# Kernel optimization log

Hardware: AMD Instinct MI355X
Metric: run time of the kernel (lower is better)

## Reference

```python
import jax, jax.numpy as jnp
import numpy as np

N = 30000      # nodes
E = 480000     # edges (before self-loops)
IN = 128       # in_dim
HID = 256      # hidden_dim
HEADS = 4
C = HID // HEADS  # per-head channels = 64
NEG_SLOPE = 0.2


def setup_inputs() -> dict:
    key = jax.random.key(0)
    ks = jax.random.split(key, 12)
    s_in = 1.0 / np.sqrt(IN)
    s_h = 1.0 / np.sqrt(HID)
    return {
        "x": jax.random.normal(ks[0], (N, IN), dtype=jnp.float32),
        "edge_index": jax.random.randint(ks[1], (2, E), 0, N, dtype=jnp.int32),
        # GAT layer 1 (in: IN -> HEADS*C)
        "W1": jax.random.normal(ks[2], (IN, HID), dtype=jnp.float32) * s_in,
        "att_src1": jax.random.normal(ks[3], (HEADS, C), dtype=jnp.float32) * s_h,
        "att_dst1": jax.random.normal(ks[4], (HEADS, C), dtype=jnp.float32) * s_h,
        "b1": jnp.zeros((HID,), dtype=jnp.float32),
        # GAT layer 2 (in: HID -> HEADS*C)
        "W2": jax.random.normal(ks[5], (HID, HID), dtype=jnp.float32) * s_h,
        "att_src2": jax.random.normal(ks[6], (HEADS, C), dtype=jnp.float32) * s_h,
        "att_dst2": jax.random.normal(ks[7], (HEADS, C), dtype=jnp.float32) * s_h,
        "b2": jnp.zeros((HID,), dtype=jnp.float32),
        # LayerNorms
        "g1": jnp.ones((HID,), dtype=jnp.float32),
        "be1": jnp.zeros((HID,), dtype=jnp.float32),
        "g2": jnp.ones((HID,), dtype=jnp.float32),
        "be2": jnp.zeros((HID,), dtype=jnp.float32),
        # residual projection (in_dim != hidden_dim)
        "Wp": jax.random.normal(ks[8], (IN, HID), dtype=jnp.float32) * s_in,
        "bp": jnp.zeros((HID,), dtype=jnp.float32),
    }


def layer_norm(x, g, b, eps=1e-5):
    mu = jnp.mean(x, axis=-1, keepdims=True)
    var = jnp.var(x, axis=-1, keepdims=True)
    return (x - mu) * jax.lax.rsqrt(var + eps) * g + b


def gat_conv(x, src, dst, W, a_src, a_dst, bias):
    """PyG-style GATConv (concat heads). src/dst already include self-loops."""
    n = x.shape[0]
    h = (x @ W).reshape(n, HEADS, C)                     # (N, H, C)
    e_src = jnp.sum(h * a_src, axis=-1)                  # (N, H)
    e_dst = jnp.sum(h * a_dst, axis=-1)                  # (N, H)
    e = jax.nn.leaky_relu(e_src[src] + e_dst[dst], NEG_SLOPE)  # (Etot, H)
    # per-destination segment softmax (numerically stable)
    e_max = jax.lax.stop_gradient(jax.ops.segment_max(e, dst, num_segments=n))
    p = jnp.exp(e - e_max[dst])
    denom = jax.ops.segment_sum(p, dst, num_segments=n)[dst]
    alpha = p / denom                                    # (Etot, H)
    out = jax.ops.segment_sum(h[src] * alpha[..., None], dst, num_segments=n)
    return out.reshape(n, HID) + bias


def reference(x, edge_index, W1, att_src1, att_dst1, b1, W2, att_src2, att_dst2, b2,
              g1, be1, g2, be2, Wp, bp):
    n = x.shape[0]
    loop = jnp.arange(n, dtype=edge_index.dtype)
    src = jnp.concatenate([edge_index[0], loop])
    dst = jnp.concatenate([edge_index[1], loop])

    residual = x @ Wp + bp                               # proj residual
    h = gat_conv(x, src, dst, W1, att_src1, att_dst1, b1)
    h = jax.nn.elu(layer_norm(h + residual, g1, be1))
    # dropout is identity at inference
    residual = h
    h2 = gat_conv(h, src, dst, W2, att_src2, att_dst2, b2)
    out = jax.nn.elu(layer_norm(h2 + residual, g2, be2))
    return out
```

## Files before the change

kernel.cpp:

```cpp
#include <hip/hip_runtime.h>
#include <cstdint>
#include <cstddef>

#define N_NODES 30000
#define E_EDGES 480000
#define ETOT    510000
#define IN_DIM  128
#define HID     256
#define HEADS   4
#define NEG_SLOPE 0.2f
#define DEG_BLOCKS 1993

static inline int cdiv(int a, int b){ return (a + b - 1) / b; }

typedef short bf16x8 __attribute__((ext_vector_type(8)));
typedef float f32x4  __attribute__((ext_vector_type(4)));
typedef float f32x2  __attribute__((ext_vector_type(2)));

__device__ __forceinline__ unsigned short f2bf(float f) {
  unsigned u = __float_as_uint(f);
  unsigned r = (u + 0x7FFFu + ((u >> 16) & 1u)) >> 16;
  return (unsigned short)r;
}
__device__ __forceinline__ float bf2f(unsigned short s) {
  return __uint_as_float((unsigned)s << 16);
}
__device__ __forceinline__ unsigned char f2fp8(float v) {
  return (unsigned char)(__builtin_amdgcn_cvt_pk_fp8_f32(v, v, 0, false) & 0xFF);
}

__global__ __launch_bounds__(256) void zero_deg(int4* __restrict__ deg4)
{
  deg4[blockIdx.x * 256 + threadIdx.x] = int4{0, 0, 0, 0};
}

__global__ __launch_bounds__(256) void setup(
    const int* __restrict__ ei, int* __restrict__ deg,
    const float* __restrict__ x, const float* __restrict__ W1,
    const float* __restrict__ Wp, const float* __restrict__ W2,
    ushort* __restrict__ xbf, ushort* __restrict__ w1t,
    ushort* __restrict__ wpt, ushort* __restrict__ w2t)
{
  int b = blockIdx.x;
  int t = threadIdx.x;
  if (b < DEG_BLOCKS) {
    int e = b * 256 + t;
    if (e < ETOT) {
      int d = (e < E_EDGES) ? ei[E_EDGES + e] : (e - E_EDGES);
      atomicAdd(&deg[d], 1);
    }
    return;
  }
  b -= DEG_BLOCKS;
  if (b < 3750) {
    int i = b * 256 + t;
    float4 v = ((const float4*)x)[i];
    ushort4 o;
    o.x = f2bf(v.x); o.y = f2bf(v.y); o.z = f2bf(v.z); o.w = f2bf(v.w);
    ((ushort4*)xbf)[i] = o;
  } else if (b < 3750 + 128) {
    int k = b - 3750;
    w1t[(size_t)t * IN_DIM + k] = f2bf(W1[(size_t)k * HID + t]);
  } else if (b < 3750 + 256) {
    int k = b - 3878;
    wpt[(size_t)t * IN_DIM + k] = f2bf(Wp[(size_t)k * HID + t]);
  } else {
    int k = b - 4006;
    w2t[(size_t)t * HID + k] = f2bf(W2[(size_t)k * HID + t]);
  }
}

template<int K, bool L1>
__global__ __launch_bounds__(256) void gemm_fused(
    const ushort* __restrict__ A,
    const ushort* __restrict__ WT,
    const float* __restrict__ att_src, const float* __restrict__ att_dst,
    unsigned char* __restrict__ hout, float* __restrict__ esrc, float* __restrict__ edst,
    ushort* __restrict__ rout, const float* __restrict__ pbias, int n)
{
  const int wave = threadIdx.x >> 6;
  const int lane = threadIdx.x & 63;
  const int wr = wave >> 1, wc = wave & 1;
  const int brow = blockIdx.x * 128 + wr * 64;
  const int bcol = blockIdx.y * 128 + wc * 64;
  const int lrow = lane & 15;
  const int kgrp = lane >> 4;

  f32x4 acc[4][4] = {};
  for (int k0 = 0; k0 < K; k0 += 32) {
    const int kb = k0 + kgrp * 8;
    bf16x8 a[4], b[4];
    #pragma unroll
    for (int mi = 0; mi < 4; ++mi) {
      int r = brow + mi * 16 + lrow;
      r = min(r, n - 1);
      a[mi] = *(const bf16x8*)&A[(size_t)r * K + kb];
    }
    #pragma unroll
    for (int ni = 0; ni < 4; ++ni) {
      int c = bcol + ni * 16 + lrow;
      b[ni] = *(const bf16x8*)&WT[(size_t)c * K + kb];
    }
    #pragma unroll
    for (int mi = 0; mi < 4; ++mi)
      #pragma unroll
      for (int ni = 0; ni < 4; ++ni)
        acc[mi][ni] = __builtin_amdgcn_mfma_f32_16x16x32_bf16(a[mi], b[ni], acc[mi][ni], 0, 0, 0);
  }
  const bool proj = L1 && (bcol >= 256);
  #pragma unroll
  for (int mi = 0; mi < 4; ++mi) {
    #pragma unroll
    for (int r = 0; r < 4; ++r) {
      int row = brow + mi * 16 + kgrp * 4 + r;
      if (row < n) {
        #pragma unroll
        for (int ni = 0; ni < 4; ++ni) {
          int colg = bcol + ni * 16 + lrow;
          float v = acc[mi][ni][r];
          if (proj) {
            int c = colg - 256;
            rout[(size_t)row * HID + c] = f2bf(v + pbias[c]);
          } else {
            hout[(size_t)row * HID + colg] = f2fp8(v);
          }
        }
      }
    }
  }
  if (!proj) {
    const int hh = bcol >> 6;
    float as[4], ad[4];
    #pragma unroll
    for (int ni = 0; ni < 4; ++ni) {
      as[ni] = att_src[hh * 64 + ni * 16 + lrow];
      ad[ni] = att_dst[hh * 64 + ni * 16 + lrow];
    }
    #pragma unroll
    for (int mi = 0; mi < 4; ++mi) {
      #pragma unroll
      for (int r = 0; r < 4; ++r) {
        float vs = 0.f, vd = 0.f;
        #pragma unroll
        for (int ni = 0; ni < 4; ++ni) {
          float c = acc[mi][ni][r];
          vs += c * as[ni];
          vd += c * ad[ni];
        }
        #pragma unroll
        for (int m = 1; m <= 8; m <<= 1) {
          vs += __shfl_xor(vs, m);
          vd += __shfl_xor(vd, m);
        }
        int row = brow + mi * 16 + kgrp * 4 + r;
        if (lrow == 0 && row < n) {
          esrc[row * HEADS + hh] = vs;
          edst[row * HEADS + hh] = vd;
        }
      }
    }
  }
}

__global__ __launch_bounds__(1024) void scan_rowptr(const int* __restrict__ deg,
                                                    int* __restrict__ rowptr,
                                                    int* __restrict__ cursor)
{
  const int CE = 30;
  __shared__ int sc[1024];
  int t = threadIdx.x;
  int base = t * CE;
  int local[CE];
  int s = 0;
  #pragma unroll
  for (int i = 0; i < CE; ++i) {
    int idx = base + i;
    int v = (idx < N_NODES) ? deg[idx] : 0;
    local[i] = s;
    s += v;
  }
  sc[t] = s;
  __syncthreads();
  for (int o = 1; o < 1024; o <<= 1) {
    int v = (t >= o) ? sc[t - o] : 0;
    __syncthreads();
    sc[t] += v;
    __syncthreads();
  }
  int off = sc[t] - s;
  #pragma unroll
  for (int i = 0; i < CE; ++i) {
    int idx = base + i;
    if (idx < N_NODES) {
      rowptr[idx] = off + local[i];
      cursor[idx] = off + local[i];
    }
  }
  if (t == 1023) rowptr[N_NODES] = off + s;
}

__global__ __launch_bounds__(256) void scatter_edges(const int* __restrict__ ei,
                                                     int* __restrict__ cursor,
                                                     int* __restrict__ col)
{
  int e = blockIdx.x * blockDim.x + threadIdx.x;
  if (e >= ETOT) return;
  int s, d;
  if (e < E_EDGES) { s = ei[e]; d = ei[E_EDGES + e]; }
  else             { s = d = e - E_EDGES; }
  int pos = atomicAdd(&cursor[d], 1);
  col[pos] = s;
}

template<bool WRITE_BF16>
__global__ __launch_bounds__(256) void gat_agg(
    const int* __restrict__ rowptr, const int* __restrict__ col,
    const float* __restrict__ esrc, const float* __restrict__ edst,
    const unsigned char* __restrict__ h8, const float* __restrict__ bias,
    const ushort* __restrict__ resid, const float* __restrict__ gamma,
    const float* __restrict__ beta, float* __restrict__ out_f32,
    ushort* __restrict__ out_bf16)
{
  const int t = threadIdx.x;
  const int lane16 = t & 15;
  const int d = blockIdx.x * 16 + (t >> 4);
  const int cblk = lane16 * 16;
  const int headc = lane16 >> 2;
  const int r0 = rowptr[d], r1 = rowptr[d + 1];

  const float edh = edst[d * HEADS + headc];
  f32x2 acc2[8] = {};
  float dp = 0.f;

  for (int j = r0; j < r1; j += 8) {
    int s[8];
    #pragma unroll
    for (int i = 0; i < 8; ++i) s[i] = col[min(j + i, r1 - 1)];
    float es[8];
    #pragma unroll
    for (int i = 0; i < 8; ++i) es[i] = esrc[s[i] * HEADS + headc];
    uint4 w[8];
    #pragma unroll
    for (int i = 0; i < 8; ++i)
      w[i] = *(const uint4*)&h8[(size_t)s[i] * HID + cblk];
    #pragma unroll
    for (int i = 0; i < 8; ++i) {
      float v = es[i] + edh;
      v = (v >= 0.f) ? v : NEG_SLOPE * v;
      float p = (j + i < r1) ? __expf(v) : 0.f;
      dp += p;
      f32x2 p2 = { p, p };
      unsigned wd0 = w[i].x, wd1 = w[i].y, wd2 = w[i].z, wd3 = w[i].w;
      acc2[0] += __builtin_amdgcn_cvt_pk_f32_fp8(wd0, false) * p2;
      acc2[1] += __builtin_amdgcn_cvt_pk_f32_fp8(wd0, true)  * p2;
      acc2[2] += __builtin_amdgcn_cvt_pk_f32_fp8(wd1, false) * p2;
      acc2[3] += __builtin_amdgcn_cvt_pk_f32_fp8(wd1, true)  * p2;
      acc2[4] += __builtin_amdgcn_cvt_pk_f32_fp8(wd2, false) * p2;
      acc2[5] += __builtin_amdgcn_cvt_pk_f32_fp8(wd2, true)  * p2;
      acc2[6] += __builtin_amdgcn_cvt_pk_f32_fp8(wd3, false) * p2;
      acc2[7] += __builtin_amdgcn_cvt_pk_f32_fp8(wd3, true)  * p2;
    }
  }

  float rden = 1.f / dp;

  f32x2 v2[8];
  {
    const uint4* rp = (const uint4*)&resid[(size_t)d * HID + cblk];
    uint4 r0v = rp[0], r1v = rp[1];
    unsigned rd[8] = { r0v.x, r0v.y, r0v.z, r0v.w, r1v.x, r1v.y, r1v.z, r1v.w };
    const f32x2* b2 = (const f32x2*)&bias[cblk];
    f32x2 rden2 = { rden, rden };
    #pragma unroll
    for (int q = 0; q < 8; ++q) {
      f32x2 rw;
      rw.x = __uint_as_float(rd[q] << 16);
      rw.y = __uint_as_float(rd[q] & 0xffff0000u);
      v2[q] = acc2[q] * rden2 + b2[q] + rw;
    }
  }

  float s1 = 0.f, s2 = 0.f;
  #pragma unroll
  for (int q = 0; q < 8; ++q) {
    s1 += v2[q].x + v2[q].y;
    s2 += v2[q].x * v2[q].x + v2[q].y * v2[q].y;
  }
  #pragma unroll
  for (int m = 1; m <= 8; m <<= 1) {
    s1 += __shfl_xor(s1, m);
    s2 += __shfl_xor(s2, m);
  }
  float mu = s1 * (1.f / HID);
  float var = s2 * (1.f / HID) - mu * mu;
  float rr = rsqrtf(var + 1e-5f);

  const f32x2* g2 = (const f32x2*)&gamma[cblk];
  const f32x2* e2 = (const f32x2*)&beta[cblk];
  float y[16];
  #pragma unroll
  for (int q = 0; q < 8; ++q) {
    f32x2 g = g2[q], e = e2[q];
    float t0 = (v2[q].x - mu) * rr * g.x + e.x;
    float t1 = (v2[q].y - mu) * rr * g.y + e.y;
    y[2 * q]     = (t0 > 0.f) ? t0 : expm1f(t0);
    y[2 * q + 1] = (t1 > 0.f) ? t1 : expm1f(t1);
  }
  if (WRITE_BF16) {
    uint4 o[2];
    #pragma unroll
    for (int q = 0; q < 8; ++q) {
      unsigned wv = (unsigned)f2bf(y[2 * q]) | ((unsigned)f2bf(y[2 * q + 1]) << 16);
      ((unsigned*)o)[q] = wv;
    }
    uint4* op = (uint4*)&out_bf16[(size_t)d * HID + cblk];
    op[0] = o[0]; op[1] = o[1];
  } else {
    float4* op = (float4*)&out_f32[(size_t)d * HID + cblk];
    #pragma unroll
    for (int q = 0; q < 4; ++q) {
      float4 ov = { y[4 * q], y[4 * q + 1], y[4 * q + 2], y[4 * q + 3] };
      op[q] = ov;
    }
  }
}

extern "C" void kernel_launch(void* const* d_in, const int* in_sizes, int n_in,
                              void* d_out, int out_size, void* d_ws, size_t ws_size,
                              hipStream_t stream) {
  const float* x   = (const float*)d_in[0];
  const int*   ei  = (const int*)d_in[1];
  const float* W1  = (const float*)d_in[2];
  const float* as1 = (const float*)d_in[3];
  const float* ad1 = (const float*)d_in[4];
  const float* b1  = (const float*)d_in[5];
  const float* W2  = (const float*)d_in[6];
  const float* as2 = (const float*)d_in[7];
  const float* ad2 = (const float*)d_in[8];
  const float* b2  = (const float*)d_in[9];
  const float* g1  = (const float*)d_in[10];
  const float* be1 = (const float*)d_in[11];
  const float* g2  = (const float*)d_in[12];
  const float* be2 = (const float*)d_in[13];
  const float* Wp  = (const float*)d_in[14];
  const float* bp  = (const float*)d_in[15];
  float* out = (float*)d_out;

  const size_t NB16 = (size_t)N_NODES * HID * sizeof(ushort);
  const size_t NB8  = (size_t)N_NODES * HID;
  const size_t XB16 = (size_t)N_NODES * IN_DIM * sizeof(ushort);
  const size_t NH_BUF = (size_t)N_NODES * HEADS * sizeof(float);
  char* ws = (char*)d_ws;
  size_t off = 0;
  unsigned char* h8 = (unsigned char*)(ws + off); off += NB8;
  ushort* hAbf  = (ushort*)(ws + off); off += NB16;
  ushort* rbf   = (ushort*)(ws + off); off += NB16;
  ushort* xbf   = (ushort*)(ws + off); off += XB16;
  ushort* w1t   = (ushort*)(ws + off); off += (size_t)HID * IN_DIM * 2;
  ushort* wpt   = (ushort*)(ws + off); off += (size_t)HID * IN_DIM * 2;
  ushort* w2t   = (ushort*)(ws + off); off += (size_t)HID * HID * 2;
  float*  esrc  = (float*) (ws + off); off += NH_BUF;
  float*  edstb = (float*) (ws + off); off += NH_BUF;
  int*    deg    = (int*)(ws + off); off += (size_t)30720 * 4;
  int*    rowptr = (int*)(ws + off); off += (size_t)(N_NODES + 1) * 4;
  int*    cursor = (int*)(ws + off); off += (size_t)N_NODES * 4;
  int*    col    = (int*)(ws + off); off += (size_t)ETOT * 4;

  zero_deg<<<30, 256, 0, stream>>>((int4*)deg);
  setup<<<DEG_BLOCKS + 3750 + 128 + 128 + 256, 256, 0, stream>>>(
      ei, deg, x, W1, Wp, W2, xbf, w1t, wpt, w2t);
  scan_rowptr<<<1, 1024, 0, stream>>>(deg, rowptr, cursor);
  scatter_edges<<<cdiv(ETOT, 256), 256, 0, stream>>>(ei, cursor, col);

  gemm_fused<IN_DIM, true><<<dim3(cdiv(N_NODES, 128), 4), 256, 0, stream>>>(
      xbf, w1t, as1, ad1, h8, esrc, edstb, rbf, bp, N_NODES);
  gat_agg<true><<<N_NODES / 16, 256, 0, stream>>>(
      rowptr, col, esrc, edstb, h8, b1, rbf, g1, be1, nullptr, hAbf);

  gemm_fused<HID, false><<<dim3(cdiv(N_NODES, 128), 2), 256, 0, stream>>>(
      hAbf, w2t, as2, ad2, h8, esrc, edstb, nullptr, nullptr, N_NODES);
  gat_agg<false><<<N_NODES / 16, 256, 0, stream>>>(
      rowptr, col, esrc, edstb, h8, b2, hAbf, g2, be2, out, nullptr);
}
```

Measured before the change: 218.3 us.

## Fuse edge scatter into first GEMM launch, warp-shuffle scan, hoist residual load

```diff
diff --git a/kernel.cpp b/kernel.cpp
--- a/kernel.cpp
+++ b/kernel.cpp
@@ -10,6 +10,7 @@
 #define HEADS   4
 #define NEG_SLOPE 0.2f
 #define DEG_BLOCKS 1993
+#define GEMM1_BX 235
 
 static inline int cdiv(int a, int b){ return (a + b - 1) / b; }
 
@@ -71,7 +72,8 @@
 }
 
 template<int K, bool L1>
-__global__ __launch_bounds__(256) void gemm_fused(
+__device__ __forceinline__ void gemm_body(
+    int bx, int by,
     const ushort* __restrict__ A,
     const ushort* __restrict__ WT,
     const float* __restrict__ att_src, const float* __restrict__ att_dst,
@@ -81,8 +83,8 @@
   const int wave = threadIdx.x >> 6;
   const int lane = threadIdx.x & 63;
   const int wr = wave >> 1, wc = wave & 1;
-  const int brow = blockIdx.x * 128 + wr * 64;
-  const int bcol = blockIdx.y * 128 + wc * 64;
+  const int brow = bx * 128 + wr * 64;
+  const int bcol = by * 128 + wc * 64;
   const int lrow = lane & 15;
   const int kgrp = lane >> 4;
 
@@ -162,13 +164,50 @@
   }
 }
 
+__global__ __launch_bounds__(256) void gemm1_scatter(
+    const int* __restrict__ ei, int* __restrict__ cursor, int* __restrict__ col,
+    const ushort* __restrict__ A, const ushort* __restrict__ WT,
+    const float* __restrict__ att_src, const float* __restrict__ att_dst,
+    unsigned char* __restrict__ hout, float* __restrict__ esrc,
+    float* __restrict__ edst, ushort* __restrict__ rout,
+    const float* __restrict__ pbias, int n)
+{
+  int b = blockIdx.x;
+  if (b < DEG_BLOCKS) {
+    int e = b * 256 + threadIdx.x;
+    if (e < ETOT) {
+      int s, d;
+      if (e < E_EDGES) { s = ei[e]; d = ei[E_EDGES + e]; }
+      else             { s = d = e - E_EDGES; }
+      int pos = atomicAdd(&cursor[d], 1);
+      col[pos] = s;
+    }
+    return;
+  }
+  b -= DEG_BLOCKS;
+  gemm_body<IN_DIM, true>(b % GEMM1_BX, b / GEMM1_BX,
+                          A, WT, att_src, att_dst, hout, esrc, edst, rout, pbias, n);
+}
+
+__global__ __launch_bounds__(256) void gemm2(
+    const ushort* __restrict__ A, const ushort* __restrict__ WT,
+    const float* __restrict__ att_src, const float* __restrict__ att_dst,
+    unsigned char* __restrict__ hout, float* __restrict__ esrc,
+    float* __restrict__ edst, int n)
+{
+  gemm_body<HID, false>(blockIdx.x, blockIdx.y,
+                        A, WT, att_src, att_dst, hout, esrc, edst, nullptr, nullptr, n);
+}
+
 __global__ __launch_bounds__(1024) void scan_rowptr(const int* __restrict__ deg,
                                                     int* __restrict__ rowptr,
                                                     int* __restrict__ cursor)
 {
   const int CE = 30;
-  __shared__ int sc[1024];
+  __shared__ int wtot[16];
+  __shared__ int wexc[16];
   int t = threadIdx.x;
+  int wv = t >> 6, lane = t & 63;
   int base = t * CE;
   int local[CE];
   int s = 0;
@@ -179,37 +218,35 @@
     local[i] = s;
     s += v;
   }
-  sc[t] = s;
+  int incl = s;
+  #pragma unroll
+  for (int off = 1; off < 64; off <<= 1) {
+    int v = __shfl_up(incl, off);
+    if (lane >= off) incl += v;
+  }
+  if (lane == 63) wtot[wv] = incl;
   __syncthreads();
-  for (int o = 1; o < 1024; o <<= 1) {
-    int v = (t >= o) ? sc[t - o] : 0;
-    __syncthreads();
-    sc[t] += v;
-    __syncthreads();
-  }
-  int off = sc[t] - s;
+  if (t < 16) {
+    int v = wtot[t];
+    int inc2 = v;
+    #pragma unroll
+    for (int off = 1; off < 16; off <<= 1) {
+      int u = __shfl_up(inc2, off);
+      if (t >= off) inc2 += u;
+    }
+    wexc[t] = inc2 - v;
+  }
+  __syncthreads();
+  int off0 = wexc[wv] + (incl - s);
   #pragma unroll
   for (int i = 0; i < CE; ++i) {
     int idx = base + i;
     if (idx < N_NODES) {
-      rowptr[idx] = off + local[i];
-      cursor[idx] = off + local[i];
-    }
-  }
-  if (t == 1023) rowptr[N_NODES] = off + s;
-}
-
-__global__ __launch_bounds__(256) void scatter_edges(const int* __restrict__ ei,
-                                                     int* __restrict__ cursor,
-                                                     int* __restrict__ col)
-{
-  int e = blockIdx.x * blockDim.x + threadIdx.x;
-  if (e >= ETOT) return;
-  int s, d;
-  if (e < E_EDGES) { s = ei[e]; d = ei[E_EDGES + e]; }
-  else             { s = d = e - E_EDGES; }
-  int pos = atomicAdd(&cursor[d], 1);
-  col[pos] = s;
+      rowptr[idx] = off0 + local[i];
+      cursor[idx] = off0 + local[i];
+    }
+  }
+  if (t == 1023) rowptr[N_NODES] = off0 + s;
 }
 
 template<bool WRITE_BF16>
@@ -228,7 +265,10 @@
   const int headc = lane16 >> 2;
   const int r0 = rowptr[d], r1 = rowptr[d + 1];
 
+  const uint4* rp = (const uint4*)&resid[(size_t)d * HID + cblk];
+  uint4 r0v = rp[0], r1v = rp[1];
   const float edh = edst[d * HEADS + headc];
+
   f32x2 acc2[8] = {};
   float dp = 0.f;
 
@@ -266,8 +306,6 @@
 
   f32x2 v2[8];
   {
-    const uint4* rp = (const uint4*)&resid[(size_t)d * HID + cblk];
-    uint4 r0v = rp[0], r1v = rp[1];
     unsigned rd[8] = { r0v.x, r0v.y, r0v.z, r0v.w, r1v.x, r1v.y, r1v.z, r1v.w };
     const f32x2* b2 = (const f32x2*)&bias[cblk];
     f32x2 rden2 = { rden, rden };
@@ -370,15 +408,14 @@
   setup<<<DEG_BLOCKS + 3750 + 128 + 128 + 256, 256, 0, stream>>>(
       ei, deg, x, W1, Wp, W2, xbf, w1t, wpt, w2t);
   scan_rowptr<<<1, 1024, 0, stream>>>(deg, rowptr, cursor);
-  scatter_edges<<<cdiv(ETOT, 256), 256, 0, stream>>>(ei, cursor, col);
-
-  gemm_fused<IN_DIM, true><<<dim3(cdiv(N_NODES, 128), 4), 256, 0, stream>>>(
-      xbf, w1t, as1, ad1, h8, esrc, edstb, rbf, bp, N_NODES);
+
+  gemm1_scatter<<<DEG_BLOCKS + GEMM1_BX * 4, 256, 0, stream>>>(
+      ei, cursor, col, xbf, w1t, as1, ad1, h8, esrc, edstb, rbf, bp, N_NODES);
   gat_agg<true><<<N_NODES / 16, 256, 0, stream>>>(
       rowptr, col, esrc, edstb, h8, b1, rbf, g1, be1, nullptr, hAbf);
 
-  gemm_fused<HID, false><<<dim3(cdiv(N_NODES, 128), 2), 256, 0, stream>>>(
-      hAbf, w2t, as2, ad2, h8, esrc, edstb, nullptr, nullptr, N_NODES);
+  gemm2<<<dim3(GEMM1_BX, 2), 256, 0, stream>>>(
+      hAbf, w2t, as2, ad2, h8, esrc, edstb, N_NODES);
   gat_agg<false><<<N_NODES / 16, 256, 0, stream>>>(
       rowptr, col, esrc, edstb, h8, b2, hAbf, g2, be2, out, nullptr);
 }
```

New measurement: 217.8 us. No clear change (-0.3%).
